# Kernel tuning notes

Hardware: AMD Instinct MI355X
Metric: run time of the kernel (lower is better)

Reference implementation:

```python
import jax, jax.numpy as jnp
import numpy as np
import math

EMBED = 1024
HEADS = 16
HEAD_DIM = EMBED // HEADS
B, S = 2, 2048


def setup_inputs() -> dict:
    key = jax.random.key(0)
    ks = jax.random.split(key, 11)
    s = 1.0 / math.sqrt(EMBED)
    return {
        "query": jax.random.normal(ks[0], (B, S, EMBED), jnp.float32),
        "key_": jax.random.normal(ks[1], (B, S, EMBED), jnp.float32),
        "value": jax.random.normal(ks[2], (B, S, EMBED), jnp.float32),
        "Wq": jax.random.normal(ks[3], (EMBED, EMBED), jnp.float32) * s,
        "bq": jax.random.normal(ks[4], (EMBED,), jnp.float32) * s,
        "Wk": jax.random.normal(ks[5], (EMBED, EMBED), jnp.float32) * s,
        "bk": jax.random.normal(ks[6], (EMBED,), jnp.float32) * s,
        "Wv": jax.random.normal(ks[7], (EMBED, EMBED), jnp.float32) * s,
        "bv": jax.random.normal(ks[8], (EMBED,), jnp.float32) * s,
        "Wo": jax.random.normal(ks[9], (EMBED, EMBED), jnp.float32) * s,
        "bo": jax.random.normal(ks[10], (EMBED,), jnp.float32) * s,
    }


def reference(query, key_, value, Wq, bq, Wk, bk, Wv, bv, Wo, bo):
    b, s, e = query.shape
    # projections (torch Linear: x @ W.T + b)
    q = query @ Wq.T + bq
    k = key_ @ Wk.T + bk
    v = value @ Wv.T + bv
    # [B, H, S, hd]
    q = q.reshape(b, s, HEADS, HEAD_DIM).transpose(0, 2, 1, 3)
    k = k.reshape(b, s, HEADS, HEAD_DIM).transpose(0, 2, 1, 3)
    v = v.reshape(b, s, HEADS, HEAD_DIM).transpose(0, 2, 1, 3)
    scores = jnp.einsum("bhqd,bhkd->bhqk", q, k) / math.sqrt(HEAD_DIM)
    attn = jax.nn.softmax(scores, axis=-1)
    out = jnp.einsum("bhqk,bhkd->bhqd", attn, v)
    out = out.transpose(0, 2, 1, 3).reshape(b, s, e)
    return out @ Wo.T + bo
```

## Files before the change

### kernel.cpp

```cpp
#include <hip/hip_runtime.h>
#include <hip/hip_bf16.h>

using bf16_t = __bf16;
using bf16x4 = __attribute__((ext_vector_type(4))) __bf16;
using bf16x8 = __attribute__((ext_vector_type(8))) __bf16;
using f32x4  = __attribute__((ext_vector_type(4))) float;
using u32 = unsigned int;

constexpr int S_ = 2048, E_ = 1024, M_ = 4096;
constexpr size_t MAT_A = (size_t)M_ * E_;
constexpr size_t MAT_W = (size_t)E_ * E_;

__device__ __forceinline__ bf16_t tobf(float f) {
  unsigned u = __builtin_bit_cast(unsigned, f);
  unsigned short r = (unsigned short)((u + 0x7fffu + ((u >> 16) & 1u)) >> 16);
  return __builtin_bit_cast(bf16_t, r);
}
__device__ __forceinline__ u32 packbf2(float a, float b) {
  u32 ua = __builtin_bit_cast(u32, a) + 0x8000u;
  u32 ub = __builtin_bit_cast(u32, b) + 0x8000u;
  return (ua >> 16) | (ub & 0xffff0000u);
}
__device__ __forceinline__ void async_lds16(const bf16_t* g, bf16_t* l) {
  __builtin_amdgcn_global_load_lds(
      (const __attribute__((address_space(1))) unsigned int*)g,
      (__attribute__((address_space(3))) unsigned int*)l, 16, 0, 0);
}

__global__ __launch_bounds__(256) void cvt7(
    const float* __restrict__ s0, const float* __restrict__ s1,
    const float* __restrict__ s2, const float* __restrict__ s3,
    const float* __restrict__ s4, const float* __restrict__ s5,
    const float* __restrict__ s6,
    bf16_t* __restrict__ d0, bf16_t* __restrict__ d1,
    bf16_t* __restrict__ d2, bf16_t* __restrict__ d3,
    bf16_t* __restrict__ d4, bf16_t* __restrict__ d5,
    bf16_t* __restrict__ d6) {
  const int w = blockIdx.y;
  const size_t n = w < 3 ? MAT_A : MAT_W;
  size_t i = ((size_t)blockIdx.x * 256 + threadIdx.x) * 8;
  if (i >= n) return;
  const float* s = w == 0 ? s0 : w == 1 ? s1 : w == 2 ? s2 : w == 3 ? s3
                 : w == 4 ? s4 : w == 5 ? s5 : s6;
  bf16_t* d = w == 0 ? d0 : w == 1 ? d1 : w == 2 ? d2 : w == 3 ? d3
            : w == 4 ? d4 : w == 5 ? d5 : d6;
  float4 a = *(const float4*)(s + i);
  float4 b = *(const float4*)(s + i + 4);
  bf16x8 o;
  o[0] = tobf(a.x); o[1] = tobf(a.y); o[2] = tobf(a.z); o[3] = tobf(a.w);
  o[4] = tobf(b.x); o[5] = tobf(b.y); o[6] = tobf(b.z); o[7] = tobf(b.w);
  *(bf16x8*)(d + i) = o;
}

__global__ __launch_bounds__(256) void gemm_qkv(
    const bf16_t* __restrict__ xq, const bf16_t* __restrict__ xk,
    const bf16_t* __restrict__ xv, const bf16_t* __restrict__ wq,
    const bf16_t* __restrict__ wk, const bf16_t* __restrict__ wv,
    const float* __restrict__ bq, const float* __restrict__ bk,
    const float* __restrict__ bv, bf16_t* __restrict__ outb,
    bf16_t* __restrict__ Vt) {
  constexpr int K = 1024, N = 1024, BK = 32;
  constexpr float SC = 0.18033688011f;
  __shared__ __align__(16) bf16_t As[128 * BK];
  __shared__ __align__(16) bf16_t Bs[128 * BK];
  const int which = blockIdx.y >> 3;
  const bf16_t* X = which == 0 ? xq : which == 1 ? xk : xv;
  const bf16_t* W = which == 0 ? wq : which == 1 ? wk : wv;
  const float* bias = which == 0 ? bq : which == 1 ? bk : bv;
  const int row0 = blockIdx.x * 128, col0 = (blockIdx.y & 7) * 128;

  const int tid = threadIdx.x, lane = tid & 63, wave = tid >> 6;
  const int l15 = lane & 15, q = lane >> 4;
  const int wm = (wave & 1) * 64, wn = (wave >> 1) * 64;
  const f32x4 fzero = {0.f, 0.f, 0.f, 0.f};

  f32x4 acc[4][4];
#pragma unroll
  for (int i = 0; i < 4; ++i)
#pragma unroll
    for (int j = 0; j < 4; ++j) acc[i][j] = fzero;

  const bf16_t* gA = X + (size_t)(row0 + wave * 32 + (lane >> 2)) * K + (lane & 3) * 8;
  const bf16_t* gB = W + (size_t)(col0 + wave * 32 + (lane >> 2)) * K + (lane & 3) * 8;
  bf16_t* lA = As + wave * 32 * BK;
  bf16_t* lB = Bs + wave * 32 * BK;

  for (int k0 = 0; k0 < K; k0 += BK) {
    __syncthreads();
    async_lds16(gA + k0, lA);
    async_lds16(gA + k0 + 16 * K, lA + 16 * BK);
    async_lds16(gB + k0, lB);
    async_lds16(gB + k0 + 16 * K, lB + 16 * BK);
    __syncthreads();
    bf16x8 af[4], bw[4];
#pragma unroll
    for (int i = 0; i < 4; ++i)
      af[i] = *(const bf16x8*)(As + (wm + i * 16 + l15) * BK + q * 8);
#pragma unroll
    for (int j = 0; j < 4; ++j)
      bw[j] = *(const bf16x8*)(Bs + (wn + j * 16 + l15) * BK + q * 8);
#pragma unroll
    for (int i = 0; i < 4; ++i)
#pragma unroll
      for (int j = 0; j < 4; ++j)
        acc[i][j] = __builtin_amdgcn_mfma_f32_16x16x32_bf16(af[i], bw[j],
                                                            acc[i][j], 0, 0, 0);
  }

  if (which < 2) {
    const float sc = which == 0 ? SC : 1.0f;
    bf16_t* C = outb + (size_t)which * MAT_A;
#pragma unroll
    for (int j = 0; j < 4; ++j) {
      const int col = col0 + wn + j * 16 + l15;
      const float bc = bias[col];
#pragma unroll
      for (int i = 0; i < 4; ++i)
#pragma unroll
        for (int r = 0; r < 4; ++r) {
          const int row = row0 + wm + i * 16 + q * 4 + r;
          C[(size_t)row * N + col] = tobf((acc[i][j][r] + bc) * sc);
        }
    }
  } else {
#pragma unroll
    for (int j = 0; j < 4; ++j) {
      const int col = col0 + wn + j * 16 + l15;
      const float bc = bias[col];
      const int head = col >> 6, d = col & 63;
#pragma unroll
      for (int i = 0; i < 4; ++i) {
        const int row = row0 + wm + i * 16 + q * 4;
        const int bb = row >> 11, tok = row & 2047;
        bf16x4 o;
#pragma unroll
        for (int r = 0; r < 4; ++r) o[r] = tobf(acc[i][j][r] + bc);
        *(bf16x4*)(Vt + ((size_t)(bb * 16 + head) * 64 + d) * S_ + tok) = o;
      }
    }
  }
}

__global__ __launch_bounds__(256) void gemm_o(const bf16_t* __restrict__ X,
                                              const bf16_t* __restrict__ W,
                                              const float* __restrict__ bias,
                                              float* __restrict__ C) {
  constexpr int K = 1024, N = 1024, BK = 32;
  __shared__ __align__(16) bf16_t As[64 * BK];
  __shared__ __align__(16) bf16_t Bs[128 * BK];
  const int tid = threadIdx.x, lane = tid & 63, wave = tid >> 6;
  const int l15 = lane & 15, q = lane >> 4;
  const int row0 = blockIdx.x * 64, col0 = blockIdx.y * 128;
  const int wm = (wave & 1) * 32, wn = (wave >> 1) * 64;
  const f32x4 fzero = {0.f, 0.f, 0.f, 0.f};

  f32x4 acc[2][4];
#pragma unroll
  for (int i = 0; i < 2; ++i)
#pragma unroll
    for (int j = 0; j < 4; ++j) acc[i][j] = fzero;

  const bf16_t* gA = X + (size_t)(row0 + wave * 16 + (lane >> 2)) * K + (lane & 3) * 8;
  const bf16_t* gB = W + (size_t)(col0 + wave * 32 + (lane >> 2)) * K + (lane & 3) * 8;
  bf16_t* lA = As + wave * 16 * BK;
  bf16_t* lB = Bs + wave * 32 * BK;

  for (int k0 = 0; k0 < K; k0 += BK) {
    __syncthreads();
    async_lds16(gA + k0, lA);
    async_lds16(gB + k0, lB);
    async_lds16(gB + k0 + 16 * K, lB + 16 * BK);
    __syncthreads();
    bf16x8 af[2], bw[4];
#pragma unroll
    for (int i = 0; i < 2; ++i)
      af[i] = *(const bf16x8*)(As + (wm + i * 16 + l15) * BK + q * 8);
#pragma unroll
    for (int j = 0; j < 4; ++j)
      bw[j] = *(const bf16x8*)(Bs + (wn + j * 16 + l15) * BK + q * 8);
#pragma unroll
    for (int i = 0; i < 2; ++i)
#pragma unroll
      for (int j = 0; j < 4; ++j)
        acc[i][j] = __builtin_amdgcn_mfma_f32_16x16x32_bf16(af[i], bw[j],
                                                            acc[i][j], 0, 0, 0);
  }

#pragma unroll
  for (int j = 0; j < 4; ++j) {
    const int col = col0 + wn + j * 16 + l15;
    const float bc = bias[col];
#pragma unroll
    for (int i = 0; i < 2; ++i)
#pragma unroll
      for (int r = 0; r < 4; ++r) {
        const int row = row0 + wm + i * 16 + q * 4 + r;
        C[(size_t)row * N + col] = acc[i][j][r] + bc;
      }
  }
}

__global__ __launch_bounds__(256) void attn_mfma(
    const bf16_t* __restrict__ Qm, const bf16_t* __restrict__ Km,
    const bf16_t* __restrict__ Vtg, bf16_t* __restrict__ Om) {
  constexpr int LDP = 72;
  __shared__ __align__(16) bf16_t Ks[2][64 * 64];
  __shared__ __align__(16) bf16_t Vs[2][64 * 64];
  __shared__ __align__(16) bf16_t Ps[4][2][16 * LDP];

  const int tid = threadIdx.x, lane = tid & 63, wave = tid >> 6;
  const int l15 = lane & 15, q = lane >> 4;
  const int bh = blockIdx.x & 31, qb = blockIdx.x >> 5;
  const int b = bh >> 4, h = bh & 15;
  const size_t rowbase = (size_t)b * S_;
  const int hcol = h * 64;
  const int q0 = qb * 128 + wave * 32;

  const int srow = lane >> 3;
  const int schunk = (lane & 7) ^ srow;
  const bf16_t* gK = Km + (rowbase + wave * 16 + srow) * E_ + hcol + schunk * 8;
  const bf16_t* gV = Vtg + ((size_t)bh * 64 + wave * 16 + srow) * S_ + schunk * 8;

  bf16x8 qf[2][2];
#pragma unroll
  for (int qt = 0; qt < 2; ++qt) {
    const bf16_t* qp = Qm + (rowbase + q0 + qt * 16 + l15) * E_ + hcol + q * 8;
    qf[qt][0] = *(const bf16x8*)qp;
    qf[qt][1] = *(const bf16x8*)(qp + 32);
  }

  const f32x4 fzero = {0.f, 0.f, 0.f, 0.f};
  f32x4 oacc[2][4];
#pragma unroll
  for (int qt = 0; qt < 2; ++qt)
#pragma unroll
    for (int mt = 0; mt < 4; ++mt) oacc[qt][mt] = fzero;
  float lsum[2] = {0.f, 0.f};

  const int rbase = l15 * 64;
  int ck[2];
  ck[0] = ((q) ^ (l15 & 7)) * 8;
  ck[1] = ((4 + q) ^ (l15 & 7)) * 8;
  bf16_t* pw0 = Ps[wave][0] + l15 * LDP;
  bf16_t* pw1 = Ps[wave][1] + l15 * LDP;

  async_lds16(gK, Ks[0] + wave * 1024);
  async_lds16(gK + (size_t)8 * E_, Ks[0] + wave * 1024 + 512);
  async_lds16(gV, Vs[0] + wave * 1024);
  async_lds16(gV + (size_t)8 * S_, Vs[0] + wave * 1024 + 512);

  for (int t = 0; t < 32; ++t) {
    const int pb = t & 1;
    __syncthreads();
    if (t + 1 < 32) {
      const size_t koff = (size_t)((t + 1) * 64) * E_;
      const int voff = (t + 1) * 64;
      bf16_t* dK = Ks[pb ^ 1] + wave * 1024;
      bf16_t* dV = Vs[pb ^ 1] + wave * 1024;
      async_lds16(gK + koff, dK);
      async_lds16(gK + koff + (size_t)8 * E_, dK + 512);
      async_lds16(gV + voff, dV);
      async_lds16(gV + voff + (size_t)8 * S_, dV + 512);
    }
    const bf16_t* Kbuf = Ks[pb];
    const bf16_t* Vbuf = Vs[pb];

#pragma unroll
    for (int nt = 0; nt < 4; ++nt) {
      bf16x8 a0 = *(const bf16x8*)(Kbuf + nt * 1024 + rbase + ck[0]);
      bf16x8 a1 = *(const bf16x8*)(Kbuf + nt * 1024 + rbase + ck[1]);
#pragma unroll
      for (int qt = 0; qt < 2; ++qt) {
        f32x4 st = fzero;
        st = __builtin_amdgcn_mfma_f32_16x16x32_bf16(a0, qf[qt][0], st, 0, 0, 0);
        st = __builtin_amdgcn_mfma_f32_16x16x32_bf16(a1, qf[qt][1], st, 0, 0, 0);
        float p0 = __builtin_amdgcn_exp2f(st[0]);
        float p1 = __builtin_amdgcn_exp2f(st[1]);
        float p2 = __builtin_amdgcn_exp2f(st[2]);
        float p3 = __builtin_amdgcn_exp2f(st[3]);
        lsum[qt] += (p0 + p1) + (p2 + p3);
        uint2 pk;
        pk.x = packbf2(p0, p1);
        pk.y = packbf2(p2, p3);
        *(uint2*)((qt ? pw1 : pw0) + nt * 16 + q * 4) = pk;
      }
    }

#pragma unroll
    for (int kk = 0; kk < 2; ++kk) {
      bf16x8 bp0 = *(const bf16x8*)(pw0 + kk * 32 + q * 8);
      bf16x8 bp1 = *(const bf16x8*)(pw1 + kk * 32 + q * 8);
#pragma unroll
      for (int mt = 0; mt < 4; ++mt) {
        bf16x8 av = *(const bf16x8*)(Vbuf + mt * 1024 + rbase + ck[kk]);
        oacc[0][mt] = __builtin_amdgcn_mfma_f32_16x16x32_bf16(av, bp0,
                                                              oacc[0][mt], 0, 0, 0);
        oacc[1][mt] = __builtin_amdgcn_mfma_f32_16x16x32_bf16(av, bp1,
                                                              oacc[1][mt], 0, 0, 0);
      }
    }
  }

#pragma unroll
  for (int qt = 0; qt < 2; ++qt) {
    float l = lsum[qt];
    l += __shfl_xor(l, 16);
    l += __shfl_xor(l, 32);
    const float inv = 1.0f / l;
    const size_t orow = (rowbase + q0 + qt * 16 + l15) * E_ + hcol + q * 4;
#pragma unroll
    for (int mt = 0; mt < 4; ++mt) {
      bf16x4 o;
#pragma unroll
      for (int r = 0; r < 4; ++r) o[r] = tobf(oacc[qt][mt][r] * inv);
      *(bf16x4*)(Om + orow + mt * 16) = o;
    }
  }
}

extern "C" void kernel_launch(void* const* d_in, const int* in_sizes, int n_in,
                              void* d_out, int out_size, void* d_ws, size_t ws_size,
                              hipStream_t stream) {
  const float* query = (const float*)d_in[0];
  const float* key_  = (const float*)d_in[1];
  const float* value = (const float*)d_in[2];
  const float* Wq = (const float*)d_in[3];
  const float* bq = (const float*)d_in[4];
  const float* Wk = (const float*)d_in[5];
  const float* bk = (const float*)d_in[6];
  const float* Wv = (const float*)d_in[7];
  const float* bv = (const float*)d_in[8];
  const float* Wo = (const float*)d_in[9];
  const float* bo = (const float*)d_in[10];

  bf16_t* qc  = (bf16_t*)d_ws;
  bf16_t* kc  = qc + MAT_A;
  bf16_t* vc  = kc + MAT_A;
  bf16_t* wqb = vc + MAT_A;
  bf16_t* wkb = wqb + MAT_W;
  bf16_t* wvb = wkb + MAT_W;
  bf16_t* wob = wvb + MAT_W;
  bf16_t* Qb  = wob + MAT_W;
  bf16_t* Kb  = Qb + MAT_A;
  bf16_t* Vt  = Kb + MAT_A;
  bf16_t* AOb = Vt + MAT_A;

  cvt7<<<dim3(MAT_A / 2048, 7), 256, 0, stream>>>(
      query, key_, value, Wq, Wk, Wv, Wo,
      qc, kc, vc, wqb, wkb, wvb, wob);
  gemm_qkv<<<dim3(32, 24), 256, 0, stream>>>(qc, kc, vc, wqb, wkb, wvb,
                                             bq, bk, bv, Qb, Vt);
  attn_mfma<<<512, 256, 0, stream>>>(Qb, Kb, Vt, AOb);
  gemm_o<<<dim3(64, 8), 256, 0, stream>>>(AOb, wob, bo, (float*)d_out);
}
```

Before: 238.9 us.

## Widen GEMM K-tiles with swizzled LDS, stage V transpose, MFMA row sums

```diff
diff --git a/kernel.cpp b/kernel.cpp
--- a/kernel.cpp
+++ b/kernel.cpp
@@ -27,7 +27,7 @@
       (__attribute__((address_space(3))) unsigned int*)l, 16, 0, 0);
 }
 
-__global__ __launch_bounds__(256) void cvt7(
+__global__ __launch_bounds__(256) void cvt_all(
     const float* __restrict__ s0, const float* __restrict__ s1,
     const float* __restrict__ s2, const float* __restrict__ s3,
     const float* __restrict__ s4, const float* __restrict__ s5,
@@ -36,20 +36,28 @@
     bf16_t* __restrict__ d2, bf16_t* __restrict__ d3,
     bf16_t* __restrict__ d4, bf16_t* __restrict__ d5,
     bf16_t* __restrict__ d6) {
-  const int w = blockIdx.y;
-  const size_t n = w < 3 ? MAT_A : MAT_W;
-  size_t i = ((size_t)blockIdx.x * 256 + threadIdx.x) * 8;
-  if (i >= n) return;
-  const float* s = w == 0 ? s0 : w == 1 ? s1 : w == 2 ? s2 : w == 3 ? s3
-                 : w == 4 ? s4 : w == 5 ? s5 : s6;
-  bf16_t* d = w == 0 ? d0 : w == 1 ? d1 : w == 2 ? d2 : w == 3 ? d3
-            : w == 4 ? d4 : w == 5 ? d5 : d6;
-  float4 a = *(const float4*)(s + i);
-  float4 b = *(const float4*)(s + i + 4);
+  size_t i8 = ((size_t)blockIdx.x * 256 + threadIdx.x) * 8;
+  const float* s;
+  bf16_t* d;
+  size_t off;
+  if (i8 < 3 * MAT_A) {
+    int w = (int)(i8 >> 22);
+    off = i8 & (MAT_A - 1);
+    s = w == 0 ? s0 : w == 1 ? s1 : s2;
+    d = w == 0 ? d0 : w == 1 ? d1 : d2;
+  } else {
+    size_t j = i8 - 3 * MAT_A;
+    int w = (int)(j >> 20);
+    off = j & (MAT_W - 1);
+    s = w == 0 ? s3 : w == 1 ? s4 : w == 2 ? s5 : s6;
+    d = w == 0 ? d3 : w == 1 ? d4 : w == 2 ? d5 : d6;
+  }
+  float4 a = *(const float4*)(s + off);
+  float4 b = *(const float4*)(s + off + 4);
   bf16x8 o;
   o[0] = tobf(a.x); o[1] = tobf(a.y); o[2] = tobf(a.z); o[3] = tobf(a.w);
   o[4] = tobf(b.x); o[5] = tobf(b.y); o[6] = tobf(b.z); o[7] = tobf(b.w);
-  *(bf16x8*)(d + i) = o;
+  *(bf16x8*)(d + off) = o;
 }
 
 __global__ __launch_bounds__(256) void gemm_qkv(
@@ -59,10 +67,12 @@
     const float* __restrict__ bq, const float* __restrict__ bk,
     const float* __restrict__ bv, bf16_t* __restrict__ outb,
     bf16_t* __restrict__ Vt) {
-  constexpr int K = 1024, N = 1024, BK = 32;
+  constexpr int K = 1024, N = 1024, BK = 64;
   constexpr float SC = 0.18033688011f;
-  __shared__ __align__(16) bf16_t As[128 * BK];
-  __shared__ __align__(16) bf16_t Bs[128 * BK];
+  __shared__ __align__(16) bf16_t smem[18432];
+  bf16_t* As = smem;
+  bf16_t* Bs = smem + 128 * BK;
+
   const int which = blockIdx.y >> 3;
   const bf16_t* X = which == 0 ? xq : which == 1 ? xk : xv;
   const bf16_t* W = which == 0 ? wq : which == 1 ? wk : wv;
@@ -80,31 +90,41 @@
 #pragma unroll
     for (int j = 0; j < 4; ++j) acc[i][j] = fzero;
 
-  const bf16_t* gA = X + (size_t)(row0 + wave * 32 + (lane >> 2)) * K + (lane & 3) * 8;
-  const bf16_t* gB = W + (size_t)(col0 + wave * 32 + (lane >> 2)) * K + (lane & 3) * 8;
+  const int srow = lane >> 3;
+  const int schunk = ((lane & 7) ^ srow) * 8;
+  const bf16_t* gA = X + (size_t)(row0 + wave * 32 + srow) * K + schunk;
+  const bf16_t* gB = W + (size_t)(col0 + wave * 32 + srow) * K + schunk;
   bf16_t* lA = As + wave * 32 * BK;
   bf16_t* lB = Bs + wave * 32 * BK;
 
+  int ck[2];
+  ck[0] = ((q) ^ (l15 & 7)) * 8;
+  ck[1] = ((4 + q) ^ (l15 & 7)) * 8;
+
   for (int k0 = 0; k0 < K; k0 += BK) {
     __syncthreads();
-    async_lds16(gA + k0, lA);
-    async_lds16(gA + k0 + 16 * K, lA + 16 * BK);
-    async_lds16(gB + k0, lB);
-    async_lds16(gB + k0 + 16 * K, lB + 16 * BK);
-    __syncthreads();
-    bf16x8 af[4], bw[4];
-#pragma unroll
-    for (int i = 0; i < 4; ++i)
-      af[i] = *(const bf16x8*)(As + (wm + i * 16 + l15) * BK + q * 8);
-#pragma unroll
-    for (int j = 0; j < 4; ++j)
-      bw[j] = *(const bf16x8*)(Bs + (wn + j * 16 + l15) * BK + q * 8);
-#pragma unroll
-    for (int i = 0; i < 4; ++i)
+#pragma unroll
+    for (int p = 0; p < 4; ++p) {
+      async_lds16(gA + k0 + (size_t)(p * 8) * K, lA + p * 8 * BK);
+      async_lds16(gB + k0 + (size_t)(p * 8) * K, lB + p * 8 * BK);
+    }
+    __syncthreads();
+#pragma unroll
+    for (int h = 0; h < 2; ++h) {
+      bf16x8 af[4], bw[4];
+#pragma unroll
+      for (int i = 0; i < 4; ++i)
+        af[i] = *(const bf16x8*)(As + (wm + i * 16 + l15) * BK + ck[h]);
 #pragma unroll
       for (int j = 0; j < 4; ++j)
-        acc[i][j] = __builtin_amdgcn_mfma_f32_16x16x32_bf16(af[i], bw[j],
-                                                            acc[i][j], 0, 0, 0);
+        bw[j] = *(const bf16x8*)(Bs + (wn + j * 16 + l15) * BK + ck[h]);
+#pragma unroll
+      for (int i = 0; i < 4; ++i)
+#pragma unroll
+        for (int j = 0; j < 4; ++j)
+          acc[i][j] = __builtin_amdgcn_mfma_f32_16x16x32_bf16(af[i], bw[j],
+                                                              acc[i][j], 0, 0, 0);
+    }
   }
 
   if (which < 2) {
@@ -123,20 +143,29 @@
         }
     }
   } else {
+    __syncthreads();
+    bf16_t* Ep = smem + wave * 4608;
 #pragma unroll
     for (int j = 0; j < 4; ++j) {
-      const int col = col0 + wn + j * 16 + l15;
-      const float bc = bias[col];
-      const int head = col >> 6, d = col & 63;
+      const float bc = bias[col0 + wn + j * 16 + l15];
+      const int nl = j * 16 + l15;
 #pragma unroll
       for (int i = 0; i < 4; ++i) {
-        const int row = row0 + wm + i * 16 + q * 4;
-        const int bb = row >> 11, tok = row & 2047;
-        bf16x4 o;
-#pragma unroll
-        for (int r = 0; r < 4; ++r) o[r] = tobf(acc[i][j][r] + bc);
-        *(bf16x4*)(Vt + ((size_t)(bb * 16 + head) * 64 + d) * S_ + tok) = o;
+        uint2 pk;
+        pk.x = packbf2(acc[i][j][0] + bc, acc[i][j][1] + bc);
+        pk.y = packbf2(acc[i][j][2] + bc, acc[i][j][3] + bc);
+        *(uint2*)(Ep + nl * 72 + i * 16 + q * 4) = pk;
       }
+    }
+    const int head = (col0 + wn) >> 6;
+    const int tok0 = row0 + wm;
+    const int bb = tok0 >> 11, tokb = tok0 & 2047;
+    const int dl = lane >> 3, ml = (lane & 7) * 8;
+#pragma unroll
+    for (int p = 0; p < 8; ++p) {
+      const int d = dl + p * 8;
+      bf16x8 v = *(const bf16x8*)(Ep + d * 72 + ml);
+      *(bf16x8*)(Vt + ((size_t)((bb * 16 + head) * 64 + d)) * S_ + tokb + ml) = v;
     }
   }
 }
@@ -145,7 +174,7 @@
                                               const bf16_t* __restrict__ W,
                                               const float* __restrict__ bias,
                                               float* __restrict__ C) {
-  constexpr int K = 1024, N = 1024, BK = 32;
+  constexpr int K = 1024, N = 1024, BK = 64;
   __shared__ __align__(16) bf16_t As[64 * BK];
   __shared__ __align__(16) bf16_t Bs[128 * BK];
   const int tid = threadIdx.x, lane = tid & 63, wave = tid >> 6;
@@ -160,30 +189,41 @@
 #pragma unroll
     for (int j = 0; j < 4; ++j) acc[i][j] = fzero;
 
-  const bf16_t* gA = X + (size_t)(row0 + wave * 16 + (lane >> 2)) * K + (lane & 3) * 8;
-  const bf16_t* gB = W + (size_t)(col0 + wave * 32 + (lane >> 2)) * K + (lane & 3) * 8;
+  const int srow = lane >> 3;
+  const int schunk = ((lane & 7) ^ srow) * 8;
+  const bf16_t* gA = X + (size_t)(row0 + wave * 16 + srow) * K + schunk;
+  const bf16_t* gB = W + (size_t)(col0 + wave * 32 + srow) * K + schunk;
   bf16_t* lA = As + wave * 16 * BK;
   bf16_t* lB = Bs + wave * 32 * BK;
 
+  int ck[2];
+  ck[0] = ((q) ^ (l15 & 7)) * 8;
+  ck[1] = ((4 + q) ^ (l15 & 7)) * 8;
+
   for (int k0 = 0; k0 < K; k0 += BK) {
     __syncthreads();
     async_lds16(gA + k0, lA);
-    async_lds16(gB + k0, lB);
-    async_lds16(gB + k0 + 16 * K, lB + 16 * BK);
-    __syncthreads();
-    bf16x8 af[2], bw[4];
-#pragma unroll
-    for (int i = 0; i < 2; ++i)
-      af[i] = *(const bf16x8*)(As + (wm + i * 16 + l15) * BK + q * 8);
-#pragma unroll
-    for (int j = 0; j < 4; ++j)
-      bw[j] = *(const bf16x8*)(Bs + (wn + j * 16 + l15) * BK + q * 8);
-#pragma unroll
-    for (int i = 0; i < 2; ++i)
+    async_lds16(gA + k0 + (size_t)8 * K, lA + 8 * BK);
+#pragma unroll
+    for (int p = 0; p < 4; ++p)
+      async_lds16(gB + k0 + (size_t)(p * 8) * K, lB + p * 8 * BK);
+    __syncthreads();
+#pragma unroll
+    for (int h = 0; h < 2; ++h) {
+      bf16x8 af[2], bw[4];
+#pragma unroll
+      for (int i = 0; i < 2; ++i)
+        af[i] = *(const bf16x8*)(As + (wm + i * 16 + l15) * BK + ck[h]);
 #pragma unroll
       for (int j = 0; j < 4; ++j)
-        acc[i][j] = __builtin_amdgcn_mfma_f32_16x16x32_bf16(af[i], bw[j],
-                                                            acc[i][j], 0, 0, 0);
+        bw[j] = *(const bf16x8*)(Bs + (wn + j * 16 + l15) * BK + ck[h]);
+#pragma unroll
+      for (int i = 0; i < 2; ++i)
+#pragma unroll
+        for (int j = 0; j < 4; ++j)
+          acc[i][j] = __builtin_amdgcn_mfma_f32_16x16x32_bf16(af[i], bw[j],
+                                                              acc[i][j], 0, 0, 0);
+    }
   }
 
 #pragma unroll
@@ -229,13 +269,18 @@
     qf[qt][1] = *(const bf16x8*)(qp + 32);
   }
 
+  bf16x8 onesv;
+#pragma unroll
+  for (int j = 0; j < 8; ++j)
+    onesv[j] = __builtin_bit_cast(bf16_t, (unsigned short)0x3F80);
+
   const f32x4 fzero = {0.f, 0.f, 0.f, 0.f};
   f32x4 oacc[2][4];
 #pragma unroll
   for (int qt = 0; qt < 2; ++qt)
 #pragma unroll
     for (int mt = 0; mt < 4; ++mt) oacc[qt][mt] = fzero;
-  float lsum[2] = {0.f, 0.f};
+  f32x4 lsacc[2] = {fzero, fzero};
 
   const int rbase = l15 * 64;
   int ck[2];
@@ -274,14 +319,9 @@
         f32x4 st = fzero;
         st = __builtin_amdgcn_mfma_f32_16x16x32_bf16(a0, qf[qt][0], st, 0, 0, 0);
         st = __builtin_amdgcn_mfma_f32_16x16x32_bf16(a1, qf[qt][1], st, 0, 0, 0);
-        float p0 = __builtin_amdgcn_exp2f(st[0]);
-        float p1 = __builtin_amdgcn_exp2f(st[1]);
-        float p2 = __builtin_amdgcn_exp2f(st[2]);
-        float p3 = __builtin_amdgcn_exp2f(st[3]);
-        lsum[qt] += (p0 + p1) + (p2 + p3);
         uint2 pk;
-        pk.x = packbf2(p0, p1);
-        pk.y = packbf2(p2, p3);
+        pk.x = packbf2(__builtin_amdgcn_exp2f(st[0]), __builtin_amdgcn_exp2f(st[1]));
+        pk.y = packbf2(__builtin_amdgcn_exp2f(st[2]), __builtin_amdgcn_exp2f(st[3]));
         *(uint2*)((qt ? pw1 : pw0) + nt * 16 + q * 4) = pk;
       }
     }
@@ -290,6 +330,8 @@
     for (int kk = 0; kk < 2; ++kk) {
       bf16x8 bp0 = *(const bf16x8*)(pw0 + kk * 32 + q * 8);
       bf16x8 bp1 = *(const bf16x8*)(pw1 + kk * 32 + q * 8);
+      lsacc[0] = __builtin_amdgcn_mfma_f32_16x16x32_bf16(onesv, bp0, lsacc[0], 0, 0, 0);
+      lsacc[1] = __builtin_amdgcn_mfma_f32_16x16x32_bf16(onesv, bp1, lsacc[1], 0, 0, 0);
 #pragma unroll
       for (int mt = 0; mt < 4; ++mt) {
         bf16x8 av = *(const bf16x8*)(Vbuf + mt * 1024 + rbase + ck[kk]);
@@ -303,10 +345,7 @@
 
 #pragma unroll
   for (int qt = 0; qt < 2; ++qt) {
-    float l = lsum[qt];
-    l += __shfl_xor(l, 16);
-    l += __shfl_xor(l, 32);
-    const float inv = 1.0f / l;
+    const float inv = 1.0f / lsacc[qt][0];
     const size_t orow = (rowbase + q0 + qt * 16 + l15) * E_ + hcol + q * 4;
 #pragma unroll
     for (int mt = 0; mt < 4; ++mt) {
@@ -345,9 +384,8 @@
   bf16_t* Vt  = Kb + MAT_A;
   bf16_t* AOb = Vt + MAT_A;
 
-  cvt7<<<dim3(MAT_A / 2048, 7), 256, 0, stream>>>(
-      query, key_, value, Wq, Wk, Wv, Wo,
-      qc, kc, vc, wqb, wkb, wvb, wob);
+  cvt_all<<<8192, 256, 0, stream>>>(query, key_, value, Wq, Wk, Wv, Wo,
+                                    qc, kc, vc, wqb, wkb, wvb, wob);
   gemm_qkv<<<dim3(32, 24), 256, 0, stream>>>(qc, kc, vc, wqb, wkb, wvb,
                                              bq, bk, bv, Qb, Vt);
   attn_mfma<<<512, 256, 0, stream>>>(Qb, Kb, Vt, AOb);
```

New measurement: 221.6 us. 7.2% less time.
